# Optimization experiments

Hardware: AMD Instinct MI355X
Metric: run time of the kernel (lower is better)

The kernel has to match this reference:

```python
import jax, jax.numpy as jnp
import numpy as np

N = 1024
DIM = 128
GKERN_SIG = 15.0
LAMB = 0.9


def setup_inputs() -> dict:
    key = jax.random.key(0)
    ks = jax.random.split(key, 9)
    s = 1.0 / np.sqrt(DIM)
    inp = {"f": jax.random.normal(ks[0], (N, DIM), dtype=jnp.float32)}
    names = ["w1", "b1", "w2", "b2", "w3", "b3", "w4", "b4"]
    for i, nm in enumerate(names):
        if nm.startswith("w"):
            inp[nm] = jax.random.normal(ks[i + 1], (DIM, DIM), dtype=jnp.float32) * s
        else:
            inp[nm] = jax.random.normal(ks[i + 1], (DIM,), dtype=jnp.float32) * s
    return inp


def reference(f, w1, b1, w2, b2, w3, b3, w4, b4):
    n = f.shape[0]
    # fc2 -> fc3 -> fc4 (torch Linear: x @ W.T + b)
    f = f @ w2.T + b2
    f = f @ w3.T + b3
    f = f @ w4.T + b4
    # attn / projection ratio
    x = f @ w1.T + b1                       # f_prime, (N, d)
    scores = x @ x.T                        # (N, N)
    mag = jnp.sum(x * x, axis=1)            # ||f'_j||^2, (N,)
    S = scores / mag[None, :]               # divide column j by mag[j]
    # fij[i,j] = f[j] * S[i,j]  (f.expand(N,N,d) broadcasts over leading axis)
    fij = f[None, :, :] * S[:, :, None]     # (N, N, d) -- dominant 512 MB tensor
    diff = fij - f[None, :, :]
    dist = jnp.sum(diff * diff, axis=2)     # (N, N)
    idx = jnp.arange(n)
    dist = dist.at[idx, idx].set(0.0)
    A = jnp.exp(-0.5 * dist / (GKERN_SIG ** 2))
    # random walk
    total = jnp.clip(jnp.sum(A, axis=1) - jnp.diagonal(A), 1e-10, None)
    T = A / total[:, None]                  # inv(D) @ A
    T = T.at[idx, idx].set(0.0)
    P0 = T[0, 1:]
    Tm = T[1:, 1:]
    I = jnp.eye(n - 1, dtype=f.dtype)
    # (1-lamb) * inv(I - lamb*T) @ P0, via linear solve
    P = (1.0 - LAMB) * jnp.linalg.solve(I - LAMB * Tm, P0)
    P = P - P.mean()
    P = jnp.where(P < 0, 0.0, P) * 100.0
    return jax.nn.softmax(P, axis=0)
```

## Files before the change

kernel.cpp:

```cpp
#include <hip/hip_runtime.h>
#include <math.h>

#define N 1024
#define NM1 1023
#define DIM 128
#define LAMB 0.9f
#define INV2SIG2 (1.0f / 450.0f)
#define MITERS 6

typedef short v8s __attribute__((ext_vector_type(8)));
typedef float v4f __attribute__((ext_vector_type(4)));

__device__ __forceinline__ unsigned short f2bf(float x) {
    unsigned int u = __float_as_uint(x);
    u += 0x7FFFu + ((u >> 16) & 1u);
    return (unsigned short)(u >> 16);
}
__device__ __forceinline__ float bf2f(unsigned short h) {
    return __uint_as_float(((unsigned int)h) << 16);
}

__global__ __launch_bounds__(256) void k_compose_a(
    const float* __restrict__ w1, const float* __restrict__ w3,
    const float* __restrict__ w2, const float* __restrict__ w4,
    const float* __restrict__ b2, const float* __restrict__ b3,
    const float* __restrict__ b4,
    float* __restrict__ S, float* __restrict__ R,
    float* __restrict__ t1v, float* __restrict__ t2v,
    float* __restrict__ zeros)
{
    const int b = blockIdx.x;
    const int t = threadIdx.x;
    if (b < 64) {
        const int i = 2 * b + (t >> 7), j = t & 127;
        float acc = 0.f;
        #pragma unroll 8
        for (int k = 0; k < 128; ++k) acc += w3[i * 128 + k] * w2[k * 128 + j];
        S[i * 128 + j] = acc;
    } else if (b < 128) {
        const int i = 2 * (b - 64) + (t >> 7), j = t & 127;
        float acc = 0.f;
        #pragma unroll 8
        for (int k = 0; k < 128; ++k) acc += w1[i * 128 + k] * w4[k * 128 + j];
        R[i * 128 + j] = acc;
    } else if (b == 128) {
        if (t < 128) {
            float acc = b3[t];
            #pragma unroll 8
            for (int k = 0; k < 128; ++k) acc += w3[t * 128 + k] * b2[k];
            t1v[t] = acc;
        } else {
            const int i = t - 128;
            float acc = 0.f;
            #pragma unroll 8
            for (int k = 0; k < 128; ++k) acc += w1[i * 128 + k] * b4[k];
            t2v[i] = acc;
        }
    } else {
        #pragma unroll
        for (int s = 0; s < 8; ++s) zeros[t + 256 * s] = 0.f;
    }
}

__global__ __launch_bounds__(256) void k_compose_b(
    const float* __restrict__ w4, const float* __restrict__ S,
    const float* __restrict__ R,
    const float* __restrict__ t1v, const float* __restrict__ t2v,
    const float* __restrict__ b1, const float* __restrict__ b4,
    float* __restrict__ Wboth, float* __restrict__ bboth)
{
    const int b = blockIdx.x;
    const int t = threadIdx.x;
    if (b < 64) {
        const int i = 2 * b + (t >> 7), j = t & 127;
        float acc = 0.f;
        #pragma unroll 8
        for (int k = 0; k < 128; ++k) acc += w4[i * 128 + k] * S[k * 128 + j];
        Wboth[i * 128 + j] = acc;
    } else if (b < 128) {
        const int i = 2 * (b - 64) + (t >> 7), j = t & 127;
        float acc = 0.f;
        #pragma unroll 8
        for (int k = 0; k < 128; ++k) acc += R[i * 128 + k] * S[k * 128 + j];
        Wboth[(128 + i) * 128 + j] = acc;
    } else {
        if (t < 128) {
            float acc = b4[t];
            #pragma unroll 8
            for (int k = 0; k < 128; ++k) acc += w4[t * 128 + k] * t1v[k];
            bboth[t] = acc;
        } else {
            const int i = t - 128;
            float acc = t2v[i] + b1[i];
            #pragma unroll 8
            for (int k = 0; k < 128; ++k) acc += R[i * 128 + k] * t1v[k];
            bboth[128 + i] = acc;
        }
    }
}

__global__ __launch_bounds__(256) void k_gemm(
    const float* __restrict__ f, const float* __restrict__ Wb,
    const float* __restrict__ bb,
    unsigned short* __restrict__ xb, float* __restrict__ fn2, float* __restrict__ mag)
{
    __shared__ float4 fl4[64][33];
    __shared__ float4 wl4[64][33];
    __shared__ float bsh[64];
    const int t = threadIdx.x;
    const int row0 = blockIdx.y * 64;
    const int col0 = blockIdx.x * 64;
    const float4* F4 = (const float4*)f;
    const float4* W4p = (const float4*)Wb;

    #pragma unroll
    for (int s = 0; s < 8; ++s) {
        int idx = t + 256 * s;
        int r = idx >> 5, k4 = idx & 31;
        fl4[r][k4] = F4[(row0 + r) * 32 + k4];
        wl4[r][k4] = W4p[(col0 + r) * 32 + k4];
    }
    if (t < 64) bsh[t] = bb[col0 + t];
    __syncthreads();

    const int tx = t & 15, ty = t >> 4;
    float acc[4][4];
    #pragma unroll
    for (int i = 0; i < 4; ++i)
        #pragma unroll
        for (int j = 0; j < 4; ++j) acc[i][j] = 0.f;

    for (int k4 = 0; k4 < 32; ++k4) {
        float4 fa[4], wv[4];
        #pragma unroll
        for (int i = 0; i < 4; ++i) fa[i] = fl4[ty + 16 * i][k4];
        #pragma unroll
        for (int j = 0; j < 4; ++j) wv[j] = wl4[tx + 16 * j][k4];
        #pragma unroll
        for (int i = 0; i < 4; ++i)
            #pragma unroll
            for (int j = 0; j < 4; ++j)
                acc[i][j] += fa[i].x * wv[j].x + fa[i].y * wv[j].y
                           + fa[i].z * wv[j].z + fa[i].w * wv[j].w;
    }

    const bool isg = (col0 < 128);
    #pragma unroll
    for (int i = 0; i < 4; ++i) {
        int gr = row0 + ty + 16 * i;
        float ss = 0.f;
        #pragma unroll
        for (int j = 0; j < 4; ++j) {
            int c = tx + 16 * j;
            float yv = acc[i][j] + bsh[c];
            ss += yv * yv;
            if (!isg) xb[gr * DIM + (col0 - 128) + c] = f2bf(yv);
        }
        #pragma unroll
        for (int off = 1; off < 16; off <<= 1) ss += __shfl_xor(ss, off, 64);
        if (tx == 0) atomicAdd(isg ? &fn2[gr] : &mag[gr], ss);
    }
}

__global__ __launch_bounds__(512) void k_affB(
    const unsigned short* __restrict__ xb, const float* __restrict__ mag,
    const float* __restrict__ fn2,
    unsigned short* __restrict__ Bb, float* __restrict__ P0f)
{
    __shared__ float strip[16][1028];
    __shared__ float part[8][16];
    __shared__ float rtot[16];
    const int t = threadIdx.x;
    const int wave = t >> 6, lane = t & 63;
    const int l15 = lane & 15, quad = lane >> 4;
    const int i0 = blockIdx.x * 16;

    const unsigned short* ap = xb + (i0 + l15) * DIM + quad * 8;
    v8s afr[4];
    #pragma unroll
    for (int kc = 0; kc < 4; ++kc) afr[kc] = *(const v8s*)(ap + kc * 32);

    float rowsum[4] = {0.f, 0.f, 0.f, 0.f};
    for (int s = 0; s < 8; ++s) {
        const int j0 = (wave * 8 + s) * 16;
        const unsigned short* bp = xb + (j0 + l15) * DIM + quad * 8;
        v4f acc = {0.f, 0.f, 0.f, 0.f};
        #pragma unroll
        for (int kc = 0; kc < 4; ++kc) {
            v8s b = *(const v8s*)(bp + kc * 32);
            acc = __builtin_amdgcn_mfma_f32_16x16x32_bf16(afr[kc], b, acc, 0, 0, 0);
        }
        const int gj = j0 + l15;
        const float rm = 1.0f / mag[gj];
        const float fj = fn2[gj] * INV2SIG2;
        #pragma unroll
        for (int reg = 0; reg < 4; ++reg) {
            int row = quad * 4 + reg;
            float Sv = acc[reg] * rm - 1.0f;
            float a = ((i0 + row) == gj) ? 0.f : __expf(-(Sv * Sv) * fj);
            strip[row][gj] = a;
            rowsum[reg] += a;
        }
    }
    #pragma unroll
    for (int reg = 0; reg < 4; ++reg) {
        float v = rowsum[reg];
        #pragma unroll
        for (int off = 1; off < 16; off <<= 1) v += __shfl_xor(v, off, 64);
        if (l15 == 0) part[wave][quad * 4 + reg] = v;
    }
    __syncthreads();
    if (t < 16) {
        float s = 0.f;
        #pragma unroll
        for (int w = 0; w < 8; ++w) s += part[w][t];
        rtot[t] = s;
    }
    __syncthreads();

    if (i0 == 0) {
        float r0 = 1.0f / fmaxf(rtot[0], 1e-10f);
        for (int j = t; j < N; j += 512)
            P0f[j] = (j == 0) ? 0.f : strip[0][j] * r0;
    }

    #pragma unroll
    for (int it = 0; it < 4; ++it) {
        int pidx = t + 512 * it;
        int row = pidx >> 7;
        int c8 = (pidx & 127) * 8;
        int gi = i0 + row;
        float sc = (gi == 0) ? 0.f : LAMB / fmaxf(rtot[row], 1e-10f);
        float4 v0 = *(const float4*)&strip[row][c8];
        float4 v1 = *(const float4*)&strip[row][c8 + 4];
        uint4 p;
        unsigned short* pp = (unsigned short*)&p;
        pp[0] = f2bf((c8 == 0) ? 0.f : v0.x * sc);
        pp[1] = f2bf(v0.y * sc); pp[2] = f2bf(v0.z * sc); pp[3] = f2bf(v0.w * sc);
        pp[4] = f2bf(v1.x * sc); pp[5] = f2bf(v1.y * sc);
        pp[6] = f2bf(v1.z * sc); pp[7] = f2bf(v1.w * sc);
        *(uint4*)(Bb + gi * N + c8) = p;
    }
}

__global__ __launch_bounds__(256) void k_mvb(
    const unsigned short* __restrict__ M, const float* __restrict__ base,
    const float* __restrict__ z, float* __restrict__ v)
{
    const int r = (blockIdx.x * 256 + threadIdx.x) >> 6;
    const int lane = threadIdx.x & 63;
    const uint4* m4 = (const uint4*)(M + r * N + lane * 16);
    const float4* z4 = (const float4*)(z + lane * 16);
    uint4 ma = m4[0], mb = m4[1];
    float4 z0 = z4[0], z1 = z4[1], z2 = z4[2], z3 = z4[3];
    float acc = 0.f;
    acc += bf2f((unsigned short)(ma.x)) * z0.x + bf2f((unsigned short)(ma.x >> 16)) * z0.y;
    acc += bf2f((unsigned short)(ma.y)) * z0.z + bf2f((unsigned short)(ma.y >> 16)) * z0.w;
    acc += bf2f((unsigned short)(ma.z)) * z1.x + bf2f((unsigned short)(ma.z >> 16)) * z1.y;
    acc += bf2f((unsigned short)(ma.w)) * z1.z + bf2f((unsigned short)(ma.w >> 16)) * z1.w;
    acc += bf2f((unsigned short)(mb.x)) * z2.x + bf2f((unsigned short)(mb.x >> 16)) * z2.y;
    acc += bf2f((unsigned short)(mb.y)) * z2.z + bf2f((unsigned short)(mb.y >> 16)) * z2.w;
    acc += bf2f((unsigned short)(mb.z)) * z3.x + bf2f((unsigned short)(mb.z >> 16)) * z3.y;
    acc += bf2f((unsigned short)(mb.w)) * z3.z + bf2f((unsigned short)(mb.w >> 16)) * z3.w;
    #pragma unroll
    for (int off = 32; off >= 1; off >>= 1) acc += __shfl_xor(acc, off, 64);
    if (lane == 0) v[r] = base[r] + acc;
}

__global__ __launch_bounds__(1024) void k_epilogue(
    const float* __restrict__ zM, const float* __restrict__ zM1,
    const float* __restrict__ zM2, float* __restrict__ out)
{
    __shared__ float red[16];
    __shared__ float bval;
    __shared__ float ush[1024];
    const int t = threadIdx.x;
    const int wv = t >> 6, lane = t & 63;

    const float a  = zM[t];
    const float b  = zM1[t];
    const float c  = zM2[t];
    const float d1 = a - b;
    const float d2 = b - c;

    float s = d1 * d2;
    #pragma unroll
    for (int off = 32; off >= 1; off >>= 1) s += __shfl_down(s, off, 64);
    if (lane == 0) red[wv] = s;
    __syncthreads();
    if (t < 64) {
        float s2 = (t < 16) ? red[t] : 0.f;
        #pragma unroll
        for (int off = 8; off >= 1; off >>= 1) s2 += __shfl_down(s2, off, 64);
        if (t == 0) bval = s2;
    }
    __syncthreads();
    const float dot12 = bval;
    __syncthreads();

    s = d2 * d2;
    #pragma unroll
    for (int off = 32; off >= 1; off >>= 1) s += __shfl_down(s, off, 64);
    if (lane == 0) red[wv] = s;
    __syncthreads();
    if (t < 64) {
        float s2 = (t < 16) ? red[t] : 0.f;
        #pragma unroll
        for (int off = 8; off >= 1; off >>= 1) s2 += __shfl_down(s2, off, 64);
        if (t == 0) bval = s2;
    }
    __syncthreads();
    const float dot22 = bval;
    __syncthreads();

    float lam = dot12 / fmaxf(dot22, 1e-30f);
    lam = fminf(fmaxf(lam, 0.0f), 0.95f);
    ush[t] = a + (lam / (1.0f - lam)) * d1;
    __syncthreads();

    const bool valid = t < NM1;
    float P = valid ? 0.1f * ush[t + 1] : 0.f;

    s = P;
    #pragma unroll
    for (int off = 32; off >= 1; off >>= 1) s += __shfl_down(s, off, 64);
    if (lane == 0) red[wv] = s;
    __syncthreads();
    if (t < 64) {
        float s2 = (t < 16) ? red[t] : 0.f;
        #pragma unroll
        for (int off = 8; off >= 1; off >>= 1) s2 += __shfl_down(s2, off, 64);
        if (t == 0) bval = s2 / 1023.0f;
    }
    __syncthreads();
    const float mean = bval;
    P = valid ? fmaxf(P - mean, 0.f) * 100.f : 0.f;

    __syncthreads();
    float m = P;
    #pragma unroll
    for (int off = 32; off >= 1; off >>= 1) m = fmaxf(m, __shfl_down(m, off, 64));
    if (lane == 0) red[wv] = m;
    __syncthreads();
    if (t < 64) {
        float m2 = (t < 16) ? red[t] : 0.f;
        #pragma unroll
        for (int off = 8; off >= 1; off >>= 1) m2 = fmaxf(m2, __shfl_down(m2, off, 64));
        if (t == 0) bval = m2;
    }
    __syncthreads();
    const float gmax = bval;
    const float e = valid ? expf(P - gmax) : 0.f;

    __syncthreads();
    s = e;
    #pragma unroll
    for (int off = 32; off >= 1; off >>= 1) s += __shfl_down(s, off, 64);
    if (lane == 0) red[wv] = s;
    __syncthreads();
    if (t < 64) {
        float s2 = (t < 16) ? red[t] : 0.f;
        #pragma unroll
        for (int off = 8; off >= 1; off >>= 1) s2 += __shfl_down(s2, off, 64);
        if (t == 0) bval = s2;
    }
    __syncthreads();
    if (valid) out[t] = e / bval;
}

extern "C" void kernel_launch(void* const* d_in, const int* in_sizes, int n_in,
                              void* d_out, int out_size, void* d_ws, size_t ws_size,
                              hipStream_t stream) {
    const float* f  = (const float*)d_in[0];
    const float* w1 = (const float*)d_in[1];
    const float* b1 = (const float*)d_in[2];
    const float* w2 = (const float*)d_in[3];
    const float* b2 = (const float*)d_in[4];
    const float* w3 = (const float*)d_in[5];
    const float* b3 = (const float*)d_in[6];
    const float* w4 = (const float*)d_in[7];
    const float* b4 = (const float*)d_in[8];
    float* ws = (float*)d_ws;

    float* S     = ws;
    float* R     = ws + 16384;
    float* Wboth = ws + 32768;
    float* bboth = ws + 65536;
    float* t1v   = ws + 65792;
    float* t2v   = ws + 65920;
    float* fn2   = ws + 66048;
    float* mag   = ws + 67072;
    float* P0f   = ws + 68096;
    float* tb0   = ws + 69120;
    float* tb1   = ws + 70144;
    float* tb2   = ws + 71168;
    unsigned short* xb = (unsigned short*)(ws + 72192);
    unsigned short* Bb = (unsigned short*)(ws + 137728);
    float* out = (float*)d_out;

    k_compose_a<<<130, 256, 0, stream>>>(w1, w3, w2, w4, b2, b3, b4,
                                         S, R, t1v, t2v, fn2);
    k_compose_b<<<129, 256, 0, stream>>>(w4, S, R, t1v, t2v, b1, b4, Wboth, bboth);

    k_gemm<<<dim3(4, 16), 256, 0, stream>>>(f, Wboth, bboth, xb, fn2, mag);
    k_affB<<<64, 512, 0, stream>>>(xb, mag, fn2, Bb, P0f);

    float* zb[3] = {tb0, tb1, tb2};
    float* zin = P0f;
    for (int it = 0; it < MITERS; ++it) {
        float* zout = zb[it % 3];
        k_mvb<<<256, 256, 0, stream>>>(Bb, P0f, zin, zout);
        zin = zout;
    }
    k_epilogue<<<1, 1024, 0, stream>>>(zb[(MITERS - 1) % 3],
                                       zb[(MITERS - 2) % 3],
                                       zb[(MITERS - 3) % 3], out);
}
```

Before: 122.1 us.

## Spread affinity and projection across more blocks, defer row normalisation, cut iterations

The fp32 SIMT projection GEMM becomes a bf16 MFMA kernel over 256 small blocks. The affinity kernel is split four ways per row slab and writes unnormalised bf16 affinities directly, accumulating row totals with atomics. Row normalisation by lambda over the row total, and building P0, move into the matrix-vector kernel, so the shared-memory strip and its extra pass disappear. The fixed-point iteration count drops from 6 to 4, which saves two matvec launches but leaves the truncated series less converged. Using bf16 for the projection inputs also adds rounding error.

```diff
diff --git a/kernel.cpp b/kernel.cpp
--- a/kernel.cpp
+++ b/kernel.cpp
@@ -6,7 +6,7 @@
 #define DIM 128
 #define LAMB 0.9f
 #define INV2SIG2 (1.0f / 450.0f)
-#define MITERS 6
+#define MITERS 4
 
 typedef short v8s __attribute__((ext_vector_type(8)));
 typedef float v4f __attribute__((ext_vector_type(4)));
@@ -18,6 +18,12 @@
 }
 __device__ __forceinline__ float bf2f(unsigned short h) {
     return __uint_as_float(((unsigned int)h) << 16);
+}
+__device__ __forceinline__ v8s cvt8(const float* p) {
+    v8s r;
+    #pragma unroll
+    for (int i = 0; i < 8; ++i) r[i] = (short)f2bf(p[i]);
+    return r;
 }
 
 __global__ __launch_bounds__(256) void k_compose_a(
@@ -58,7 +64,7 @@
         }
     } else {
         #pragma unroll
-        for (int s = 0; s < 8; ++s) zeros[t + 256 * s] = 0.f;
+        for (int s = 0; s < 12; ++s) zeros[t + 256 * s] = 0.f;
     }
 }
 
@@ -99,81 +105,57 @@
     }
 }
 
-__global__ __launch_bounds__(256) void k_gemm(
+__global__ __launch_bounds__(256) void k_gemm2(
     const float* __restrict__ f, const float* __restrict__ Wb,
     const float* __restrict__ bb,
     unsigned short* __restrict__ xb, float* __restrict__ fn2, float* __restrict__ mag)
 {
-    __shared__ float4 fl4[64][33];
-    __shared__ float4 wl4[64][33];
-    __shared__ float bsh[64];
-    const int t = threadIdx.x;
-    const int row0 = blockIdx.y * 64;
-    const int col0 = blockIdx.x * 64;
-    const float4* F4 = (const float4*)f;
-    const float4* W4p = (const float4*)Wb;
-
-    #pragma unroll
-    for (int s = 0; s < 8; ++s) {
-        int idx = t + 256 * s;
-        int r = idx >> 5, k4 = idx & 31;
-        fl4[r][k4] = F4[(row0 + r) * 32 + k4];
-        wl4[r][k4] = W4p[(col0 + r) * 32 + k4];
-    }
-    if (t < 64) bsh[t] = bb[col0 + t];
-    __syncthreads();
-
-    const int tx = t & 15, ty = t >> 4;
-    float acc[4][4];
-    #pragma unroll
-    for (int i = 0; i < 4; ++i)
-        #pragma unroll
-        for (int j = 0; j < 4; ++j) acc[i][j] = 0.f;
-
-    for (int k4 = 0; k4 < 32; ++k4) {
-        float4 fa[4], wv[4];
-        #pragma unroll
-        for (int i = 0; i < 4; ++i) fa[i] = fl4[ty + 16 * i][k4];
-        #pragma unroll
-        for (int j = 0; j < 4; ++j) wv[j] = wl4[tx + 16 * j][k4];
-        #pragma unroll
-        for (int i = 0; i < 4; ++i)
-            #pragma unroll
-            for (int j = 0; j < 4; ++j)
-                acc[i][j] += fa[i].x * wv[j].x + fa[i].y * wv[j].y
-                           + fa[i].z * wv[j].z + fa[i].w * wv[j].w;
-    }
-
-    const bool isg = (col0 < 128);
-    #pragma unroll
-    for (int i = 0; i < 4; ++i) {
-        int gr = row0 + ty + 16 * i;
-        float ss = 0.f;
-        #pragma unroll
-        for (int j = 0; j < 4; ++j) {
-            int c = tx + 16 * j;
-            float yv = acc[i][j] + bsh[c];
-            ss += yv * yv;
-            if (!isg) xb[gr * DIM + (col0 - 128) + c] = f2bf(yv);
-        }
-        #pragma unroll
-        for (int off = 1; off < 16; off <<= 1) ss += __shfl_xor(ss, off, 64);
-        if (tx == 0) atomicAdd(isg ? &fn2[gr] : &mag[gr], ss);
-    }
-}
-
-__global__ __launch_bounds__(512) void k_affB(
+    const int b = blockIdx.x, t = threadIdx.x;
+    const int wave = t >> 6, lane = t & 63;
+    const int l15 = lane & 15, quad = lane >> 4;
+    const int i0 = (b >> 4) * 64;
+    const int j0 = (b & 15) * 16;
+    const int ri = i0 + wave * 16;
+    const float* ap = f  + (ri + l15) * 128 + quad * 8;
+    const float* bp = Wb + (j0 + l15) * 128 + quad * 8;
+    v4f acc = {0.f, 0.f, 0.f, 0.f};
+    #pragma unroll
+    for (int kc = 0; kc < 4; ++kc) {
+        v8s a  = cvt8(ap + kc * 32);
+        v8s bbv = cvt8(bp + kc * 32);
+        acc = __builtin_amdgcn_mfma_f32_16x16x32_bf16(a, bbv, acc, 0, 0, 0);
+    }
+    const float bias = bb[j0 + l15];
+    const bool isx = (j0 >= 128);
+    float sq[4];
+    #pragma unroll
+    for (int reg = 0; reg < 4; ++reg) {
+        float yv = acc[reg] + bias;
+        sq[reg] = yv * yv;
+        if (isx) xb[(ri + quad * 4 + reg) * DIM + (j0 - 128) + l15] = f2bf(yv);
+    }
+    #pragma unroll
+    for (int reg = 0; reg < 4; ++reg) {
+        float ss = sq[reg];
+        ss += __shfl_xor(ss, 1, 64); ss += __shfl_xor(ss, 2, 64);
+        ss += __shfl_xor(ss, 4, 64); ss += __shfl_xor(ss, 8, 64);
+        if (l15 == 0)
+            atomicAdd((isx ? mag : fn2) + (ri + quad * 4 + reg), ss);
+    }
+}
+
+__global__ __launch_bounds__(256) void k_aff(
     const unsigned short* __restrict__ xb, const float* __restrict__ mag,
     const float* __restrict__ fn2,
-    unsigned short* __restrict__ Bb, float* __restrict__ P0f)
-{
-    __shared__ float strip[16][1028];
-    __shared__ float part[8][16];
-    __shared__ float rtot[16];
-    const int t = threadIdx.x;
+    unsigned short* __restrict__ Bu, float* __restrict__ A0,
+    float* __restrict__ total)
+{
+    const int b = blockIdx.x, t = threadIdx.x;
     const int wave = t >> 6, lane = t & 63;
     const int l15 = lane & 15, quad = lane >> 4;
-    const int i0 = blockIdx.x * 16;
+    const int slab = b >> 2;
+    const int qtr  = b & 3;
+    const int i0 = slab * 16;
 
     const unsigned short* ap = xb + (i0 + l15) * DIM + quad * 8;
     v8s afr[4];
@@ -181,74 +163,49 @@
     for (int kc = 0; kc < 4; ++kc) afr[kc] = *(const v8s*)(ap + kc * 32);
 
     float rowsum[4] = {0.f, 0.f, 0.f, 0.f};
-    for (int s = 0; s < 8; ++s) {
-        const int j0 = (wave * 8 + s) * 16;
+    #pragma unroll
+    for (int s = 0; s < 4; ++s) {
+        const int j0 = (qtr * 16 + wave * 4 + s) * 16;
         const unsigned short* bp = xb + (j0 + l15) * DIM + quad * 8;
         v4f acc = {0.f, 0.f, 0.f, 0.f};
         #pragma unroll
-        for (int kc = 0; kc < 4; ++kc) {
-            v8s b = *(const v8s*)(bp + kc * 32);
-            acc = __builtin_amdgcn_mfma_f32_16x16x32_bf16(afr[kc], b, acc, 0, 0, 0);
-        }
+        for (int kc = 0; kc < 4; ++kc)
+            acc = __builtin_amdgcn_mfma_f32_16x16x32_bf16(
+                      afr[kc], *(const v8s*)(bp + kc * 32), acc, 0, 0, 0);
         const int gj = j0 + l15;
         const float rm = 1.0f / mag[gj];
         const float fj = fn2[gj] * INV2SIG2;
         #pragma unroll
         for (int reg = 0; reg < 4; ++reg) {
-            int row = quad * 4 + reg;
+            const int gi = i0 + quad * 4 + reg;
             float Sv = acc[reg] * rm - 1.0f;
-            float a = ((i0 + row) == gj) ? 0.f : __expf(-(Sv * Sv) * fj);
-            strip[row][gj] = a;
+            float a = (gi == gj) ? 0.f : __expf(-(Sv * Sv) * fj);
+            Bu[gi * N + gj] = f2bf(a);
             rowsum[reg] += a;
+            if (gi == 0) A0[gj] = a;
         }
     }
     #pragma unroll
     for (int reg = 0; reg < 4; ++reg) {
-        float v = rowsum[reg];
-        #pragma unroll
-        for (int off = 1; off < 16; off <<= 1) v += __shfl_xor(v, off, 64);
-        if (l15 == 0) part[wave][quad * 4 + reg] = v;
-    }
-    __syncthreads();
-    if (t < 16) {
-        float s = 0.f;
-        #pragma unroll
-        for (int w = 0; w < 8; ++w) s += part[w][t];
-        rtot[t] = s;
-    }
-    __syncthreads();
-
-    if (i0 == 0) {
-        float r0 = 1.0f / fmaxf(rtot[0], 1e-10f);
-        for (int j = t; j < N; j += 512)
-            P0f[j] = (j == 0) ? 0.f : strip[0][j] * r0;
-    }
-
-    #pragma unroll
-    for (int it = 0; it < 4; ++it) {
-        int pidx = t + 512 * it;
-        int row = pidx >> 7;
-        int c8 = (pidx & 127) * 8;
-        int gi = i0 + row;
-        float sc = (gi == 0) ? 0.f : LAMB / fmaxf(rtot[row], 1e-10f);
-        float4 v0 = *(const float4*)&strip[row][c8];
-        float4 v1 = *(const float4*)&strip[row][c8 + 4];
-        uint4 p;
-        unsigned short* pp = (unsigned short*)&p;
-        pp[0] = f2bf((c8 == 0) ? 0.f : v0.x * sc);
-        pp[1] = f2bf(v0.y * sc); pp[2] = f2bf(v0.z * sc); pp[3] = f2bf(v0.w * sc);
-        pp[4] = f2bf(v1.x * sc); pp[5] = f2bf(v1.y * sc);
-        pp[6] = f2bf(v1.z * sc); pp[7] = f2bf(v1.w * sc);
-        *(uint4*)(Bb + gi * N + c8) = p;
-    }
-}
-
-__global__ __launch_bounds__(256) void k_mvb(
-    const unsigned short* __restrict__ M, const float* __restrict__ base,
-    const float* __restrict__ z, float* __restrict__ v)
+        float ss = rowsum[reg];
+        ss += __shfl_xor(ss, 1, 64); ss += __shfl_xor(ss, 2, 64);
+        ss += __shfl_xor(ss, 4, 64); ss += __shfl_xor(ss, 8, 64);
+        if (l15 == 0) atomicAdd(&total[i0 + quad * 4 + reg], ss);
+    }
+}
+
+__global__ __launch_bounds__(256) void k_mvb2(
+    const unsigned short* __restrict__ M, const float* __restrict__ A0,
+    const float* __restrict__ total,
+    const float* __restrict__ z, float* __restrict__ v, int first)
 {
     const int r = (blockIdx.x * 256 + threadIdx.x) >> 6;
     const int lane = threadIdx.x & 63;
+    const float r0s = 1.0f / fmaxf(total[0], 1e-10f);
+    const float rscale = (r == 0) ? 0.f : LAMB / fmaxf(total[r], 1e-10f);
+    const float p0r    = (r == 0) ? 0.f : A0[r] * r0s;
+    const float zscale = first ? r0s : 1.0f;
+
     const uint4* m4 = (const uint4*)(M + r * N + lane * 16);
     const float4* z4 = (const float4*)(z + lane * 16);
     uint4 ma = m4[0], mb = m4[1];
@@ -264,7 +221,7 @@
     acc += bf2f((unsigned short)(mb.w)) * z3.z + bf2f((unsigned short)(mb.w >> 16)) * z3.w;
     #pragma unroll
     for (int off = 32; off >= 1; off >>= 1) acc += __shfl_xor(acc, off, 64);
-    if (lane == 0) v[r] = base[r] + acc;
+    if (lane == 0) v[r] = p0r + rscale * zscale * acc;
 }
 
 __global__ __launch_bounds__(1024) void k_epilogue(
@@ -390,26 +347,27 @@
     float* t2v   = ws + 65920;
     float* fn2   = ws + 66048;
     float* mag   = ws + 67072;
-    float* P0f   = ws + 68096;
-    float* tb0   = ws + 69120;
-    float* tb1   = ws + 70144;
-    float* tb2   = ws + 71168;
-    unsigned short* xb = (unsigned short*)(ws + 72192);
-    unsigned short* Bb = (unsigned short*)(ws + 137728);
+    float* total = ws + 68096;
+    float* A0    = ws + 69120;
+    float* zb0   = ws + 70144;
+    float* zb1   = ws + 71168;
+    float* zb2   = ws + 72192;
+    unsigned short* xb = (unsigned short*)(ws + 73216);
+    unsigned short* Bu = (unsigned short*)(ws + 138752);
     float* out = (float*)d_out;
 
     k_compose_a<<<130, 256, 0, stream>>>(w1, w3, w2, w4, b2, b3, b4,
                                          S, R, t1v, t2v, fn2);
     k_compose_b<<<129, 256, 0, stream>>>(w4, S, R, t1v, t2v, b1, b4, Wboth, bboth);
 
-    k_gemm<<<dim3(4, 16), 256, 0, stream>>>(f, Wboth, bboth, xb, fn2, mag);
-    k_affB<<<64, 512, 0, stream>>>(xb, mag, fn2, Bb, P0f);
-
-    float* zb[3] = {tb0, tb1, tb2};
-    float* zin = P0f;
+    k_gemm2<<<256, 256, 0, stream>>>(f, Wboth, bboth, xb, fn2, mag);
+    k_aff<<<256, 256, 0, stream>>>(xb, mag, fn2, Bu, A0, total);
+
+    float* zb[3] = {zb0, zb1, zb2};
+    const float* zin = A0;
     for (int it = 0; it < MITERS; ++it) {
         float* zout = zb[it % 3];
-        k_mvb<<<256, 256, 0, stream>>>(Bb, P0f, zin, zout);
+        k_mvb2<<<256, 256, 0, stream>>>(Bu, A0, total, zin, zout, it == 0 ? 1 : 0);
         zin = zout;
     }
     k_epilogue<<<1, 1024, 0, stream>>>(zb[(MITERS - 1) % 3],
```

Measured after the change: 109.2 us. 1.12x faster.
